# Kernel tuning notes

Measured on AMD Instinct MI355X. Metric: run time of the kernel, lower is better.

## Reference

```python
import jax, jax.numpy as jnp
import numpy as np

B, S, H = 8, 512, 768
NH, DH = 12, 64
I = 3072
E = 8
TOPK = 2
EPS = 1e-12


def _ln(x, g, b):
    m = jnp.mean(x, axis=-1, keepdims=True)
    v = jnp.mean(jnp.square(x - m), axis=-1, keepdims=True)
    return (x - m) * jax.lax.rsqrt(v + EPS) * g + b


def setup_inputs() -> dict:
    key = jax.random.key(0)
    ks = jax.random.split(key, 20)
    s_h = 1.0 / np.sqrt(H)
    s_i = 1.0 / np.sqrt(I)
    inp = {
        "hidden_states": jax.random.normal(ks[0], (B, S, H), jnp.float32),
        "Wq": jax.random.normal(ks[1], (H, H), jnp.float32) * s_h,
        "bq": jnp.zeros((H,), jnp.float32),
        "Wk": jax.random.normal(ks[2], (H, H), jnp.float32) * s_h,
        "bk": jnp.zeros((H,), jnp.float32),
        "Wv": jax.random.normal(ks[3], (H, H), jnp.float32) * s_h,
        "bv": jnp.zeros((H,), jnp.float32),
        "Wo": jax.random.normal(ks[4], (H, H), jnp.float32) * s_h,
        "bo": jnp.zeros((H,), jnp.float32),
        "ln_attn_g": jnp.ones((H,), jnp.float32),
        "ln_attn_b": jnp.zeros((H,), jnp.float32),
        "ln_ffn_g": jnp.ones((H,), jnp.float32),
        "ln_ffn_b": jnp.zeros((H,), jnp.float32),
        "Wr": jax.random.normal(ks[5], (H, E), jnp.float32) * s_h,
        "br": jnp.zeros((E,), jnp.float32),
        "W_up": jax.random.normal(ks[6], (E, H, I), jnp.float32) * s_h,
        "b_up": jnp.zeros((E, I), jnp.float32),
        "W_new": jax.random.normal(ks[7], (E, H, I), jnp.float32) * s_h,
        "b_new": jnp.zeros((E, I), jnp.float32),
        "W_down": jax.random.normal(ks[8], (E, I, H), jnp.float32) * s_i,
        "b_down": jnp.zeros((E, H), jnp.float32),
    }
    return inp


def reference(hidden_states, Wq, bq, Wk, bk, Wv, bv, Wo, bo,
              ln_attn_g, ln_attn_b, ln_ffn_g, ln_ffn_b,
              Wr, br, W_up, b_up, W_new, b_new, W_down, b_down):
    x = hidden_states
    # --- BertSelfAttention ---
    q = (x @ Wq + bq).reshape(B, S, NH, DH).transpose(0, 2, 1, 3)
    k = (x @ Wk + bk).reshape(B, S, NH, DH).transpose(0, 2, 1, 3)
    v = (x @ Wv + bv).reshape(B, S, NH, DH).transpose(0, 2, 1, 3)
    scores = jnp.einsum("bhqd,bhkd->bhqk", q, k) / np.sqrt(DH)
    probs = jax.nn.softmax(scores, axis=-1)
    ctx = jnp.einsum("bhqk,bhkd->bhqd", probs, v)
    ctx = ctx.transpose(0, 2, 1, 3).reshape(B, S, H)
    # --- BertSelfOutput: dense + residual + LayerNorm ---
    attention_output = _ln(ctx @ Wo + bo + x, ln_attn_g, ln_attn_b)
    # --- feed_forward_chunk: LayerNorm then token top-k MoE ---
    xl = _ln(attention_output, ln_ffn_g, ln_ffn_b)
    router_logits = xl @ Wr + br                      # [B,S,E]
    router_probs = jax.nn.softmax(router_logits, axis=-1)
    topw, topi = jax.lax.top_k(router_probs, TOPK)    # [B,S,K]
    topw = topw / jnp.sum(topw, axis=-1, keepdims=True)
    gates = jnp.sum(jax.nn.one_hot(topi, E, dtype=xl.dtype) * topw[..., None], axis=-2)  # [B,S,E]
    # --- experts (BertExpert: gelu(up(x)) * new(x) -> down), dense over E ---
    up = jax.nn.gelu(jnp.einsum("bsh,ehi->ebsi", xl, W_up) + b_up[:, None, None, :], approximate=False)
    gate_h = jnp.einsum("bsh,ehi->ebsi", xl, W_new) + b_new[:, None, None, :]
    y = jnp.einsum("ebsi,eih->ebsh", up * gate_h, W_down) + b_down[:, None, None, :]
    moe_out = jnp.einsum("ebsh,bse->bsh", y, gates)
    layer_output = moe_out + attention_output
    return layer_output, router_logits
```

## Files before the change

### kernel.cpp

```cpp
#include <hip/hip_runtime.h>
#include <hip/hip_bf16.h>
#include <cmath>


constexpr int cB = 8, cS = 512, cH = 768, cNH = 12, cDH = 64, cI = 3072, cE = 8;
constexpr int cT = cB * cS;
constexpr size_t TH = (size_t)cT * cH;

typedef __hip_bfloat16 bf16;
typedef __attribute__((ext_vector_type(8))) short s8v;
typedef __attribute__((ext_vector_type(4))) float f4v;

constexpr size_t SZ_WEXP     = (size_t)cE * cI * cH / 2;
constexpr size_t OFF_WUP_T   = 0;
constexpr size_t OFF_WNEW_T  = OFF_WUP_T + SZ_WEXP;
constexpr size_t OFF_WDOWN_T = OFF_WNEW_T + SZ_WEXP;
constexpr size_t OFF_QKV     = OFF_WDOWN_T + SZ_WEXP;
constexpr size_t OFF_CTX     = OFF_QKV + 4 * TH;
constexpr size_t OFF_XLB     = OFF_CTX + TH;
constexpr size_t OFF_WGT     = OFF_XLB + TH / 2;
constexpr size_t OFF_COUNTS  = OFF_WGT + 2 * cT;
constexpr size_t OFF_LISTS   = OFF_COUNTS + 16;

__device__ __forceinline__ void glds16(const void* g, void* l) {
    __builtin_amdgcn_global_load_lds(
        (const __attribute__((address_space(1))) unsigned int*)g,
        (__attribute__((address_space(3))) unsigned int*)l, 16, 0, 0);
}

__global__ void init_counts_kernel(int* __restrict__ counts) {
    if (threadIdx.x < cE) counts[threadIdx.x] = 0;
}

__global__ __launch_bounds__(256) void transpose_bf16_kernel(
    const float* __restrict__ src, bf16* __restrict__ dst, int R, int C) {
    __shared__ float tile[64][65];
    const size_t zb = (size_t)blockIdx.z * R * C;
    const int r0 = blockIdx.y * 64, c0 = blockIdx.x * 64;
    const int t = threadIdx.x;
    const int lr = t >> 4, lc = (t & 15) * 4;
#pragma unroll
    for (int i = 0; i < 4; ++i) {
        float4 v = *(const float4*)(src + zb + (size_t)(r0 + lr + i * 16) * C + c0 + lc);
        tile[lr + i * 16][lc + 0] = v.x; tile[lr + i * 16][lc + 1] = v.y;
        tile[lr + i * 16][lc + 2] = v.z; tile[lr + i * 16][lc + 3] = v.w;
    }
    __syncthreads();
#pragma unroll
    for (int i = 0; i < 4; ++i) {
        int cr = lr + i * 16;
        bf16 o[4];
#pragma unroll
        for (int j = 0; j < 4; ++j) o[j] = (bf16)tile[lc + j][cr];
        *(uint2*)(dst + zb + (size_t)(c0 + cr) * R + r0 + lc) = *(uint2*)o;
    }
}

__device__ __forceinline__ void gemm_body(
    const float* __restrict__ A, const float* __restrict__ B,
    const float* __restrict__ bias, float* __restrict__ C,
    int N, int K, int m0, int n0) {
    __shared__ float As[16][65];
    __shared__ float Bs[16][64];
    const int tid = threadIdx.x;
    const int tx = tid & 15, ty = tid >> 4;
    const int ar = tid >> 2, ac = (tid & 3) * 4;
    const int br = tid >> 4, bc = (tid & 15) * 4;
    float acc[4][4] = {};
    for (int k0 = 0; k0 < K; k0 += 16) {
        float4 av = *(const float4*)(A + (size_t)(m0 + ar) * K + k0 + ac);
        As[ac + 0][ar] = av.x; As[ac + 1][ar] = av.y;
        As[ac + 2][ar] = av.z; As[ac + 3][ar] = av.w;
        *(float4*)&Bs[br][bc] = *(const float4*)(B + (size_t)(k0 + br) * N + n0 + bc);
        __syncthreads();
#pragma unroll
        for (int kk = 0; kk < 16; ++kk) {
            float a[4], bv[4];
#pragma unroll
            for (int i = 0; i < 4; ++i) a[i] = As[kk][ty * 4 + i];
            *(float4*)bv = *(const float4*)&Bs[kk][tx * 4];
#pragma unroll
            for (int i = 0; i < 4; ++i)
#pragma unroll
                for (int j = 0; j < 4; ++j) acc[i][j] += a[i] * bv[j];
        }
        __syncthreads();
    }
#pragma unroll
    for (int i = 0; i < 4; ++i) {
        float4 o;
        o.x = acc[i][0] + bias[n0 + tx * 4 + 0];
        o.y = acc[i][1] + bias[n0 + tx * 4 + 1];
        o.z = acc[i][2] + bias[n0 + tx * 4 + 2];
        o.w = acc[i][3] + bias[n0 + tx * 4 + 3];
        *(float4*)(C + (size_t)(m0 + ty * 4 + i) * N + n0 + tx * 4) = o;
    }
}

__global__ __launch_bounds__(256) void gemm_qkv_kernel(
    const float* __restrict__ A,
    const float* __restrict__ Wq, const float* __restrict__ Wk,
    const float* __restrict__ Wv,
    const float* __restrict__ bq, const float* __restrict__ bk,
    const float* __restrict__ bv,
    float* __restrict__ q, float* __restrict__ k, float* __restrict__ v) {
    const int z = blockIdx.z;
    const float* B = (z == 0) ? Wq : (z == 1) ? Wk : Wv;
    const float* bias = (z == 0) ? bq : (z == 1) ? bk : bv;
    float* C = (z == 0) ? q : (z == 1) ? k : v;
    gemm_body(A, B, bias, C, cH, cH, blockIdx.y * 64, blockIdx.x * 64);
}

__global__ __launch_bounds__(256) void gemm_bias_kernel(
    const float* __restrict__ A, const float* __restrict__ B,
    const float* __restrict__ bias, float* __restrict__ C,
    int M, int N, int K) {
    gemm_body(A, B, bias, C, N, K, blockIdx.y * 64, blockIdx.x * 64);
}

__global__ __launch_bounds__(256) void attn_kernel(
    const float* __restrict__ q, const float* __restrict__ k,
    const float* __restrict__ v, float* __restrict__ ctx) {
    __shared__ float sQ[64][68];
    __shared__ float sKV[64][68];
    __shared__ float sS[64][68];
    __shared__ float sM[64], sL[64], sAl[64];
    const int q0 = blockIdx.x * 64, h = blockIdx.y, b = blockIdx.z;
    const int t = threadIdx.x;
    const int lr = t >> 2, lq = (t & 3) * 16;
    {
        const float* gq = q + (size_t)(b * cS + q0 + lr) * cH + h * cDH + lq;
#pragma unroll
        for (int j = 0; j < 4; ++j) {
            float4 x = *(const float4*)(gq + j * 4);
            x.x *= 0.125f; x.y *= 0.125f; x.z *= 0.125f; x.w *= 0.125f;
            *(float4*)&sQ[lr][lq + j * 4] = x;
        }
    }
    if (t < 64) { sM[t] = -1e30f; sL[t] = 0.f; }

    const int c0 = t & 15, rr = (t >> 4) * 4;
    const int d4 = (t & 15) * 4, rp = (t >> 4) * 4;
    const int sr = t >> 2, sc = (t & 3) * 16;

    float4 o_acc[4];
#pragma unroll
    for (int i = 0; i < 4; ++i) o_acc[i] = make_float4(0.f, 0.f, 0.f, 0.f);

    for (int kt = 0; kt < 8; ++kt) {
        float4 kreg[4];
        {
            const float* gk = k + (size_t)(b * cS + kt * 64 + lr) * cH + h * cDH + lq;
#pragma unroll
            for (int j = 0; j < 4; ++j) kreg[j] = *(const float4*)(gk + j * 4);
        }
        __syncthreads();
#pragma unroll
        for (int j = 0; j < 4; ++j) *(float4*)&sKV[lr][lq + j * 4] = kreg[j];
        __syncthreads();
        float accS[4][4] = {};
#pragma unroll
        for (int d = 0; d < 64; d += 4) {
            float4 qv[4], kv[4];
#pragma unroll
            for (int i = 0; i < 4; ++i) qv[i] = *(const float4*)&sQ[rr + i][d];
#pragma unroll
            for (int j = 0; j < 4; ++j) kv[j] = *(const float4*)&sKV[c0 + 16 * j][d];
#pragma unroll
            for (int i = 0; i < 4; ++i)
#pragma unroll
                for (int j = 0; j < 4; ++j)
                    accS[i][j] += qv[i].x * kv[j].x + qv[i].y * kv[j].y +
                                  qv[i].z * kv[j].z + qv[i].w * kv[j].w;
        }
#pragma unroll
        for (int i = 0; i < 4; ++i)
#pragma unroll
            for (int j = 0; j < 4; ++j) sS[rr + i][c0 + 16 * j] = accS[i][j];
        float4 vreg[4];
        {
            const float* gv = v + (size_t)(b * cS + kt * 64 + lr) * cH + h * cDH + lq;
#pragma unroll
            for (int j = 0; j < 4; ++j) vreg[j] = *(const float4*)(gv + j * 4);
        }
        __syncthreads();
        {
            float4 s[4];
#pragma unroll
            for (int j = 0; j < 4; ++j) s[j] = *(const float4*)&sS[sr][sc + j * 4];
            float m = -1e30f;
#pragma unroll
            for (int j = 0; j < 4; ++j)
                m = fmaxf(m, fmaxf(fmaxf(s[j].x, s[j].y), fmaxf(s[j].z, s[j].w)));
            m = fmaxf(m, __shfl_xor(m, 1));
            m = fmaxf(m, __shfl_xor(m, 2));
            float m_old = sM[sr];
            float m_new = fmaxf(m_old, m);
            float sum = 0.f;
#pragma unroll
            for (int j = 0; j < 4; ++j) {
                s[j].x = __expf(s[j].x - m_new); s[j].y = __expf(s[j].y - m_new);
                s[j].z = __expf(s[j].z - m_new); s[j].w = __expf(s[j].w - m_new);
                sum += s[j].x + s[j].y + s[j].z + s[j].w;
                *(float4*)&sS[sr][sc + j * 4] = s[j];
            }
            sum += __shfl_xor(sum, 1);
            sum += __shfl_xor(sum, 2);
            if ((t & 3) == 0) {
                float alpha = __expf(m_old - m_new);
                sAl[sr] = alpha;
                sM[sr] = m_new;
                sL[sr] = sL[sr] * alpha + sum;
            }
        }
#pragma unroll
        for (int j = 0; j < 4; ++j) *(float4*)&sKV[lr][lq + j * 4] = vreg[j];
        __syncthreads();
#pragma unroll
        for (int i = 0; i < 4; ++i) {
            float al = sAl[rp + i];
            o_acc[i].x *= al; o_acc[i].y *= al; o_acc[i].z *= al; o_acc[i].w *= al;
        }
        for (int kk4 = 0; kk4 < 64; kk4 += 4) {
            float4 pv[4], vv[4];
#pragma unroll
            for (int i = 0; i < 4; ++i) pv[i] = *(const float4*)&sS[rp + i][kk4];
#pragma unroll
            for (int j = 0; j < 4; ++j) vv[j] = *(const float4*)&sKV[kk4 + j][d4];
#pragma unroll
            for (int i = 0; i < 4; ++i) {
                o_acc[i].x += pv[i].x * vv[0].x + pv[i].y * vv[1].x +
                              pv[i].z * vv[2].x + pv[i].w * vv[3].x;
                o_acc[i].y += pv[i].x * vv[0].y + pv[i].y * vv[1].y +
                              pv[i].z * vv[2].y + pv[i].w * vv[3].y;
                o_acc[i].z += pv[i].x * vv[0].z + pv[i].y * vv[1].z +
                              pv[i].z * vv[2].z + pv[i].w * vv[3].z;
                o_acc[i].w += pv[i].x * vv[0].w + pv[i].y * vv[1].w +
                              pv[i].z * vv[2].w + pv[i].w * vv[3].w;
            }
        }
    }
    __syncthreads();
#pragma unroll
    for (int i = 0; i < 4; ++i) {
        float inv = 1.0f / sL[rp + i];
        float4 o = o_acc[i];
        o.x *= inv; o.y *= inv; o.z *= inv; o.w *= inv;
        *(float4*)(ctx + (size_t)(b * cS + q0 + rp + i) * cH + h * cDH + d4) = o;
    }
}

__device__ __forceinline__ float block_reduce_sum(float v, float* red) {
#pragma unroll
    for (int o = 32; o; o >>= 1) v += __shfl_xor(v, o);
    __syncthreads();
    if ((threadIdx.x & 63) == 0) red[threadIdx.x >> 6] = v;
    __syncthreads();
    return red[0] + red[1] + red[2] + red[3];
}

__global__ __launch_bounds__(256) void ln_router_kernel(
    const float* __restrict__ dense, const float* __restrict__ resid,
    const float* __restrict__ g1, const float* __restrict__ b1,
    const float* __restrict__ g2, const float* __restrict__ b2,
    const float* __restrict__ Wr, const float* __restrict__ br,
    float* __restrict__ out, bf16* __restrict__ xlb,
    float* __restrict__ out_logits, float* __restrict__ wgt,
    int* __restrict__ counts, int* __restrict__ lists) {
    __shared__ float red[4];
    __shared__ float lred[4][8];
    const int t = blockIdx.x, tid = threadIdx.x;
    const size_t base = (size_t)t * cH;
    float v[3], s = 0.f;
#pragma unroll
    for (int i = 0; i < 3; ++i) {
        v[i] = dense[base + tid + 256 * i] + resid[base + tid + 256 * i];
        s += v[i];
    }
    const float mean = block_reduce_sum(s, red) * (1.0f / cH);
    float vs = 0.f;
#pragma unroll
    for (int i = 0; i < 3; ++i) { float d = v[i] - mean; vs += d * d; }
    const float rstd = rsqrtf(block_reduce_sum(vs, red) * (1.0f / cH) + 1e-12f);
    float a[3], s2 = 0.f;
#pragma unroll
    for (int i = 0; i < 3; ++i) {
        a[i] = (v[i] - mean) * rstd * g1[tid + 256 * i] + b1[tid + 256 * i];
        out[base + tid + 256 * i] = a[i];
        s2 += a[i];
    }
    const float mean2 = block_reduce_sum(s2, red) * (1.0f / cH);
    float vs2 = 0.f;
#pragma unroll
    for (int i = 0; i < 3; ++i) { float d = a[i] - mean2; vs2 += d * d; }
    const float rstd2 = rsqrtf(block_reduce_sum(vs2, red) * (1.0f / cH) + 1e-12f);
    float xl[3];
#pragma unroll
    for (int i = 0; i < 3; ++i) {
        xl[i] = (a[i] - mean2) * rstd2 * g2[tid + 256 * i] + b2[tid + 256 * i];
        xlb[base + tid + 256 * i] = (bf16)xl[i];
    }
    float lg[cE] = {};
#pragma unroll
    for (int i = 0; i < 3; ++i) {
        const float* wr = Wr + (size_t)(tid + 256 * i) * cE;
#pragma unroll
        for (int e = 0; e < cE; ++e) lg[e] += xl[i] * wr[e];
    }
#pragma unroll
    for (int e = 0; e < cE; ++e)
#pragma unroll
        for (int o = 32; o; o >>= 1) lg[e] += __shfl_xor(lg[e], o);
    if ((tid & 63) == 0)
#pragma unroll
        for (int e = 0; e < cE; ++e) lred[tid >> 6][e] = lg[e];
    __syncthreads();
    if (tid == 0) {
        float logits[cE];
#pragma unroll
        for (int e = 0; e < cE; ++e) {
            logits[e] = lred[0][e] + lred[1][e] + lred[2][e] + lred[3][e] + br[e];
            out_logits[(size_t)t * cE + e] = logits[e];
        }
        int i0 = 0;
        for (int e = 1; e < cE; ++e) if (logits[e] > logits[i0]) i0 = e;
        int i1 = (i0 == 0) ? 1 : 0;
        for (int e = 0; e < cE; ++e)
            if (e != i0 && logits[e] > logits[i1]) i1 = e;
        float e1 = __expf(logits[i1] - logits[i0]);
        float w0 = 1.0f / (1.0f + e1);
        float w1 = e1 * w0;
        wgt[t * 2 + 0] = w0;
        wgt[t * 2 + 1] = w1;
        int p0 = atomicAdd(&counts[i0], 1);
        lists[i0 * cT + p0] = t * 2 + 0;
        int p1 = atomicAdd(&counts[i1], 1);
        lists[i1 * cT + p1] = t * 2 + 1;
    }
}

__global__ __launch_bounds__(256) void expert_up_mfma_kernel(
    const bf16* __restrict__ xlb,
    const bf16* __restrict__ WupT, const bf16* __restrict__ WnewT,
    const float* __restrict__ b_up, const float* __restrict__ b_new,
    const int* __restrict__ counts, const int* __restrict__ lists,
    bf16* __restrict__ act) {
    const int e = blockIdx.z;
    const int cnt = counts[e];
    const int m0 = blockIdx.y * 128;
    if (m0 >= cnt) return;
    const int n0 = blockIdx.x * 128;
    __shared__ short sA[128 * 32], sB1[128 * 32], sB2[128 * 32];
    __shared__ int rowa[128];
    const int t = threadIdx.x;
    if (t < 128) {
        int idx = m0 + t;
        rowa[t] = (idx < cnt) ? lists[e * cT + idx] : -1;
    }
    __syncthreads();
    const int lane = t & 63, w = t >> 6;
    const int wm = (w >> 1) * 64, wn = (w & 1) * 64;
    const int rA0 = t >> 2, kc8 = (t & 3) * 8;
    int a0 = rowa[rA0], a1 = rowa[rA0 + 64];
    const bf16* gA0 = xlb + (size_t)(a0 < 0 ? 0 : (a0 >> 1)) * cH + kc8;
    const bf16* gA1 = xlb + (size_t)(a1 < 0 ? 0 : (a1 >> 1)) * cH + kc8;
    const bf16* B1 = WupT + (size_t)e * cI * cH;
    const bf16* B2 = WnewT + (size_t)e * cI * cH;
    const bf16* gB10 = B1 + (size_t)(n0 + rA0) * cH + kc8;
    const bf16* gB11 = B1 + (size_t)(n0 + rA0 + 64) * cH + kc8;
    const bf16* gB20 = B2 + (size_t)(n0 + rA0) * cH + kc8;
    const bf16* gB21 = B2 + (size_t)(n0 + rA0 + 64) * cH + kc8;
    short* dA0  = sA  + t * 8;      short* dA1  = sA  + (t + 256) * 8;
    short* dB10 = sB1 + t * 8;      short* dB11 = sB1 + (t + 256) * 8;
    short* dB20 = sB2 + t * 8;      short* dB21 = sB2 + (t + 256) * 8;
    f4v zero = {0.f, 0.f, 0.f, 0.f};
    f4v acc1[4][4], acc2[4][4];
#pragma unroll
    for (int i = 0; i < 4; ++i)
#pragma unroll
        for (int j = 0; j < 4; ++j) { acc1[i][j] = zero; acc2[i][j] = zero; }
    const int fr = lane & 15, kg = (lane >> 4) * 8;
    for (int kk = 0; kk < cH; kk += 32) {
        glds16(gA0, dA0);   glds16(gA1, dA1);
        glds16(gB10, dB10); glds16(gB11, dB11);
        glds16(gB20, dB20); glds16(gB21, dB21);
        __syncthreads();
        s8v af[4], bf1[4], bf2[4];
#pragma unroll
        for (int i = 0; i < 4; ++i) {
            af[i]  = *(const s8v*)(sA  + (wm + i * 16 + fr) * 32 + kg);
            bf1[i] = *(const s8v*)(sB1 + (wn + i * 16 + fr) * 32 + kg);
            bf2[i] = *(const s8v*)(sB2 + (wn + i * 16 + fr) * 32 + kg);
        }
#pragma unroll
        for (int mi = 0; mi < 4; ++mi)
#pragma unroll
            for (int ni = 0; ni < 4; ++ni) {
                acc1[mi][ni] = __builtin_amdgcn_mfma_f32_16x16x32_bf16(
                    af[mi], bf1[ni], acc1[mi][ni], 0, 0, 0);
                acc2[mi][ni] = __builtin_amdgcn_mfma_f32_16x16x32_bf16(
                    af[mi], bf2[ni], acc2[mi][ni], 0, 0, 0);
            }
        __syncthreads();
        gA0 += 32; gA1 += 32; gB10 += 32; gB11 += 32; gB20 += 32; gB21 += 32;
    }
    const int cn = lane & 15, rq = (lane >> 4) * 4;
#pragma unroll
    for (int mi = 0; mi < 4; ++mi)
#pragma unroll
        for (int r = 0; r < 4; ++r) {
            int ml = wm + mi * 16 + rq + r;
            int a = rowa[ml];
            if (a < 0) continue;
            bf16* orow = act + (size_t)a * cI + n0 + wn;
#pragma unroll
            for (int ni = 0; ni < 4; ++ni) {
                int nl = ni * 16 + cn;
                float up = acc1[mi][ni][r] + b_up[e * cI + n0 + wn + nl];
                float nw = acc2[mi][ni][r] + b_new[e * cI + n0 + wn + nl];
                float g = 0.5f * up * (1.0f + erff(up * 0.70710678118654752f));
                orow[nl] = (bf16)(g * nw);
            }
        }
}

__global__ __launch_bounds__(256) void expert_down_mfma_kernel(
    const bf16* __restrict__ act, const bf16* __restrict__ WdownT,
    const float* __restrict__ b_down,
    const int* __restrict__ counts, const int* __restrict__ lists,
    const float* __restrict__ wgt, float* __restrict__ out) {
    const int e = blockIdx.z;
    const int cnt = counts[e];
    const int m0 = blockIdx.y * 128;
    if (m0 >= cnt) return;
    const int n0 = blockIdx.x * 128;
    __shared__ short sA[128 * 32], sB[128 * 32];
    __shared__ int rowa[128];
    const int t = threadIdx.x;
    if (t < 128) {
        int idx = m0 + t;
        rowa[t] = (idx < cnt) ? lists[e * cT + idx] : -1;
    }
    __syncthreads();
    const int lane = t & 63, w = t >> 6;
    const int wm = (w >> 1) * 64, wn = (w & 1) * 64;
    const int rA0 = t >> 2, kc8 = (t & 3) * 8;
    int a0 = rowa[rA0], a1 = rowa[rA0 + 64];
    const bf16* gA0 = act + (size_t)(a0 < 0 ? 0 : a0) * cI + kc8;
    const bf16* gA1 = act + (size_t)(a1 < 0 ? 0 : a1) * cI + kc8;
    const bf16* BT = WdownT + (size_t)e * cH * cI;
    const bf16* gB0 = BT + (size_t)(n0 + rA0) * cI + kc8;
    const bf16* gB1 = BT + (size_t)(n0 + rA0 + 64) * cI + kc8;
    short* dA0 = sA + t * 8;       short* dA1 = sA + (t + 256) * 8;
    short* dB0 = sB + t * 8;       short* dB1 = sB + (t + 256) * 8;
    f4v zero = {0.f, 0.f, 0.f, 0.f};
    f4v acc[4][4];
#pragma unroll
    for (int i = 0; i < 4; ++i)
#pragma unroll
        for (int j = 0; j < 4; ++j) acc[i][j] = zero;
    const int fr = lane & 15, kg = (lane >> 4) * 8;
    for (int kk = 0; kk < cI; kk += 32) {
        glds16(gA0, dA0); glds16(gA1, dA1);
        glds16(gB0, dB0); glds16(gB1, dB1);
        __syncthreads();
        s8v af[4], bf[4];
#pragma unroll
        for (int i = 0; i < 4; ++i) af[i] = *(const s8v*)(sA + (wm + i * 16 + fr) * 32 + kg);
#pragma unroll
        for (int i = 0; i < 4; ++i) bf[i] = *(const s8v*)(sB + (wn + i * 16 + fr) * 32 + kg);
#pragma unroll
        for (int mi = 0; mi < 4; ++mi)
#pragma unroll
            for (int ni = 0; ni < 4; ++ni)
                acc[mi][ni] = __builtin_amdgcn_mfma_f32_16x16x32_bf16(
                    af[mi], bf[ni], acc[mi][ni], 0, 0, 0);
        __syncthreads();
        gA0 += 32; gA1 += 32; gB0 += 32; gB1 += 32;
    }
    const int cn = lane & 15, rq = (lane >> 4) * 4;
#pragma unroll
    for (int mi = 0; mi < 4; ++mi)
#pragma unroll
        for (int r = 0; r < 4; ++r) {
            int ml = wm + mi * 16 + rq + r;
            int a = rowa[ml];
            if (a < 0) continue;
            int token = a >> 1;
            float wv = wgt[a];
#pragma unroll
            for (int ni = 0; ni < 4; ++ni) {
                int n = n0 + wn + ni * 16 + cn;
                atomicAdd(&out[(size_t)token * cH + n],
                          wv * (acc[mi][ni][r] + b_down[e * cH + n]));
            }
        }
}

extern "C" void kernel_launch(void* const* d_in, const int* in_sizes, int n_in,
                              void* d_out, int out_size, void* d_ws, size_t ws_size,
                              hipStream_t stream) {
    const float* x      = (const float*)d_in[0];
    const float* Wq     = (const float*)d_in[1];
    const float* bq     = (const float*)d_in[2];
    const float* Wk     = (const float*)d_in[3];
    const float* bk     = (const float*)d_in[4];
    const float* Wv     = (const float*)d_in[5];
    const float* bv     = (const float*)d_in[6];
    const float* Wo     = (const float*)d_in[7];
    const float* bo     = (const float*)d_in[8];
    const float* ln1g   = (const float*)d_in[9];
    const float* ln1b   = (const float*)d_in[10];
    const float* ln2g   = (const float*)d_in[11];
    const float* ln2b   = (const float*)d_in[12];
    const float* Wr     = (const float*)d_in[13];
    const float* br     = (const float*)d_in[14];
    const float* W_up   = (const float*)d_in[15];
    const float* b_up   = (const float*)d_in[16];
    const float* W_new  = (const float*)d_in[17];
    const float* b_new  = (const float*)d_in[18];
    const float* W_down = (const float*)d_in[19];
    const float* b_down = (const float*)d_in[20];

    float* out = (float*)d_out;
    float* ws  = (float*)d_ws;

    bf16* WupT   = (bf16*)(ws + OFF_WUP_T);
    bf16* WnewT  = (bf16*)(ws + OFF_WNEW_T);
    bf16* WdownT = (bf16*)(ws + OFF_WDOWN_T);
    float* q     = ws + OFF_QKV;
    float* k     = ws + OFF_QKV + TH;
    float* v     = ws + OFF_QKV + 2 * TH;
    float* tmp   = ws + OFF_QKV + 3 * TH;
    bf16* act    = (bf16*)(ws + OFF_QKV);
    float* ctx   = ws + OFF_CTX;
    bf16* xlb    = (bf16*)(ws + OFF_XLB);
    float* wgt   = ws + OFF_WGT;
    int* counts  = (int*)(ws + OFF_COUNTS);
    int* lists   = (int*)(ws + OFF_LISTS);

    init_counts_kernel<<<1, 64, 0, stream>>>(counts);

    transpose_bf16_kernel<<<dim3(48, 12, cE), 256, 0, stream>>>(W_up, WupT, cH, cI);
    transpose_bf16_kernel<<<dim3(48, 12, cE), 256, 0, stream>>>(W_new, WnewT, cH, cI);
    transpose_bf16_kernel<<<dim3(12, 48, cE), 256, 0, stream>>>(W_down, WdownT, cI, cH);

    gemm_qkv_kernel<<<dim3(cH / 64, cT / 64, 3), 256, 0, stream>>>(
        x, Wq, Wk, Wv, bq, bk, bv, q, k, v);
    attn_kernel<<<dim3(cS / 64, cNH, cB), 256, 0, stream>>>(q, k, v, ctx);
    gemm_bias_kernel<<<dim3(cH / 64, cT / 64), 256, 0, stream>>>(ctx, Wo, bo, tmp, cT, cH, cH);
    ln_router_kernel<<<cT, 256, 0, stream>>>(
        tmp, x, ln1g, ln1b, ln2g, ln2b, Wr, br,
        out, xlb, out + TH, wgt, counts, lists);

    expert_up_mfma_kernel<<<dim3(cI / 128, cT / 128, cE), 256, 0, stream>>>(
        xlb, WupT, WnewT, b_up, b_new, counts, lists, act);
    expert_down_mfma_kernel<<<dim3(cH / 128, cT / 128, cE), 256, 0, stream>>>(
        act, WdownT, b_down, counts, lists, wgt, out);
}
```

Baseline: 1.205 ms.

## Enlarge FP32 GEMM tiles to 128x128 and narrow expert-up N tile

The FP32 SIMT GEMM used for the QKV and output projections moves from 64x64 tiles with 4x4 per-thread outputs to 128x128 tiles with 8x8 per-thread outputs. Its B tile is now loaded directly into shared memory with the async global-to-LDS copy. The larger tiles raise arithmetic intensity and cut shared-memory traffic per FLOP, at the cost of more registers and fewer blocks (e.g. 6x32x3 for QKV). Separately, the expert up/new MFMA kernel halves its N tile to 64 to launch more blocks and lower accumulator register pressure, which means each A tile is fetched more often.

```diff
diff --git a/kernel.cpp b/kernel.cpp
--- a/kernel.cpp
+++ b/kernel.cpp
@@ -56,44 +56,58 @@
     }
 }
 
-__device__ __forceinline__ void gemm_body(
+__device__ __forceinline__ void gemm_body128(
     const float* __restrict__ A, const float* __restrict__ B,
     const float* __restrict__ bias, float* __restrict__ C,
     int N, int K, int m0, int n0) {
-    __shared__ float As[16][65];
-    __shared__ float Bs[16][64];
-    const int tid = threadIdx.x;
-    const int tx = tid & 15, ty = tid >> 4;
-    const int ar = tid >> 2, ac = (tid & 3) * 4;
-    const int br = tid >> 4, bc = (tid & 15) * 4;
-    float acc[4][4] = {};
+    __shared__ float As[16 * 132];
+    __shared__ float Bs[16 * 128];
+    const int t = threadIdx.x;
+    const int tx = t & 15, ty = t >> 4;
+    const int ar = t >> 2, ac = (t & 3) * 4;
+    const int bc = (t & 31) * 4, br = t >> 5;
+    const float* gB0 = B + (size_t)br * N + n0 + bc;
+    float* dB0 = Bs + t * 4;
+    float acc[8][8] = {};
     for (int k0 = 0; k0 < K; k0 += 16) {
-        float4 av = *(const float4*)(A + (size_t)(m0 + ar) * K + k0 + ac);
-        As[ac + 0][ar] = av.x; As[ac + 1][ar] = av.y;
-        As[ac + 2][ar] = av.z; As[ac + 3][ar] = av.w;
-        *(float4*)&Bs[br][bc] = *(const float4*)(B + (size_t)(k0 + br) * N + n0 + bc);
+        float4 a0 = *(const float4*)(A + (size_t)(m0 + ar) * K + k0 + ac);
+        float4 a1 = *(const float4*)(A + (size_t)(m0 + ar + 64) * K + k0 + ac);
+        glds16(gB0, dB0);
+        glds16(gB0 + (size_t)8 * N, dB0 + 1024);
+        As[(ac + 0) * 132 + ar] = a0.x; As[(ac + 1) * 132 + ar] = a0.y;
+        As[(ac + 2) * 132 + ar] = a0.z; As[(ac + 3) * 132 + ar] = a0.w;
+        As[(ac + 0) * 132 + ar + 64] = a1.x; As[(ac + 1) * 132 + ar + 64] = a1.y;
+        As[(ac + 2) * 132 + ar + 64] = a1.z; As[(ac + 3) * 132 + ar + 64] = a1.w;
         __syncthreads();
 #pragma unroll
         for (int kk = 0; kk < 16; ++kk) {
-            float a[4], bv[4];
-#pragma unroll
-            for (int i = 0; i < 4; ++i) a[i] = As[kk][ty * 4 + i];
-            *(float4*)bv = *(const float4*)&Bs[kk][tx * 4];
-#pragma unroll
-            for (int i = 0; i < 4; ++i)
-#pragma unroll
-                for (int j = 0; j < 4; ++j) acc[i][j] += a[i] * bv[j];
-        }
-        __syncthreads();
-    }
-#pragma unroll
-    for (int i = 0; i < 4; ++i) {
-        float4 o;
-        o.x = acc[i][0] + bias[n0 + tx * 4 + 0];
-        o.y = acc[i][1] + bias[n0 + tx * 4 + 1];
-        o.z = acc[i][2] + bias[n0 + tx * 4 + 2];
-        o.w = acc[i][3] + bias[n0 + tx * 4 + 3];
-        *(float4*)(C + (size_t)(m0 + ty * 4 + i) * N + n0 + tx * 4) = o;
+            float a[8], b[8];
+            *(float4*)&a[0] = *(const float4*)&As[kk * 132 + ty * 8];
+            *(float4*)&a[4] = *(const float4*)&As[kk * 132 + ty * 8 + 4];
+            *(float4*)&b[0] = *(const float4*)&Bs[kk * 128 + tx * 4];
+            *(float4*)&b[4] = *(const float4*)&Bs[kk * 128 + tx * 4 + 64];
+#pragma unroll
+            for (int i = 0; i < 8; ++i)
+#pragma unroll
+                for (int j = 0; j < 8; ++j) acc[i][j] += a[i] * b[j];
+        }
+        __syncthreads();
+        gB0 += (size_t)16 * N;
+    }
+#pragma unroll
+    for (int i = 0; i < 8; ++i) {
+        int m = m0 + ty * 8 + i;
+        float4 o0, o1;
+        o0.x = acc[i][0] + bias[n0 + tx * 4 + 0];
+        o0.y = acc[i][1] + bias[n0 + tx * 4 + 1];
+        o0.z = acc[i][2] + bias[n0 + tx * 4 + 2];
+        o0.w = acc[i][3] + bias[n0 + tx * 4 + 3];
+        o1.x = acc[i][4] + bias[n0 + 64 + tx * 4 + 0];
+        o1.y = acc[i][5] + bias[n0 + 64 + tx * 4 + 1];
+        o1.z = acc[i][6] + bias[n0 + 64 + tx * 4 + 2];
+        o1.w = acc[i][7] + bias[n0 + 64 + tx * 4 + 3];
+        *(float4*)(C + (size_t)m * N + n0 + tx * 4) = o0;
+        *(float4*)(C + (size_t)m * N + n0 + 64 + tx * 4) = o1;
     }
 }
 
@@ -108,14 +122,14 @@
     const float* B = (z == 0) ? Wq : (z == 1) ? Wk : Wv;
     const float* bias = (z == 0) ? bq : (z == 1) ? bk : bv;
     float* C = (z == 0) ? q : (z == 1) ? k : v;
-    gemm_body(A, B, bias, C, cH, cH, blockIdx.y * 64, blockIdx.x * 64);
+    gemm_body128(A, B, bias, C, cH, cH, blockIdx.y * 128, blockIdx.x * 128);
 }
 
 __global__ __launch_bounds__(256) void gemm_bias_kernel(
     const float* __restrict__ A, const float* __restrict__ B,
     const float* __restrict__ bias, float* __restrict__ C,
     int M, int N, int K) {
-    gemm_body(A, B, bias, C, N, K, blockIdx.y * 64, blockIdx.x * 64);
+    gemm_body128(A, B, bias, C, N, K, blockIdx.y * 128, blockIdx.x * 128);
 }
 
 __global__ __launch_bounds__(256) void attn_kernel(
@@ -138,11 +152,9 @@
         }
     }
     if (t < 64) { sM[t] = -1e30f; sL[t] = 0.f; }
-
     const int c0 = t & 15, rr = (t >> 4) * 4;
     const int d4 = (t & 15) * 4, rp = (t >> 4) * 4;
     const int sr = t >> 2, sc = (t & 3) * 16;
-
     float4 o_acc[4];
 #pragma unroll
     for (int i = 0; i < 4; ++i) o_acc[i] = make_float4(0.f, 0.f, 0.f, 0.f);
@@ -349,8 +361,8 @@
     const int cnt = counts[e];
     const int m0 = blockIdx.y * 128;
     if (m0 >= cnt) return;
-    const int n0 = blockIdx.x * 128;
-    __shared__ short sA[128 * 32], sB1[128 * 32], sB2[128 * 32];
+    const int n0 = blockIdx.x * 64;
+    __shared__ short sA[128 * 32], sB1[64 * 32], sB2[64 * 32];
     __shared__ int rowa[128];
     const int t = threadIdx.x;
     if (t < 128) {
@@ -359,50 +371,48 @@
     }
     __syncthreads();
     const int lane = t & 63, w = t >> 6;
-    const int wm = (w >> 1) * 64, wn = (w & 1) * 64;
+    const int wm = (w >> 1) * 64, wn = (w & 1) * 32;
     const int rA0 = t >> 2, kc8 = (t & 3) * 8;
     int a0 = rowa[rA0], a1 = rowa[rA0 + 64];
     const bf16* gA0 = xlb + (size_t)(a0 < 0 ? 0 : (a0 >> 1)) * cH + kc8;
     const bf16* gA1 = xlb + (size_t)(a1 < 0 ? 0 : (a1 >> 1)) * cH + kc8;
     const bf16* B1 = WupT + (size_t)e * cI * cH;
     const bf16* B2 = WnewT + (size_t)e * cI * cH;
-    const bf16* gB10 = B1 + (size_t)(n0 + rA0) * cH + kc8;
-    const bf16* gB11 = B1 + (size_t)(n0 + rA0 + 64) * cH + kc8;
-    const bf16* gB20 = B2 + (size_t)(n0 + rA0) * cH + kc8;
-    const bf16* gB21 = B2 + (size_t)(n0 + rA0 + 64) * cH + kc8;
-    short* dA0  = sA  + t * 8;      short* dA1  = sA  + (t + 256) * 8;
-    short* dB10 = sB1 + t * 8;      short* dB11 = sB1 + (t + 256) * 8;
-    short* dB20 = sB2 + t * 8;      short* dB21 = sB2 + (t + 256) * 8;
+    const bf16* gB1 = B1 + (size_t)(n0 + rA0) * cH + kc8;
+    const bf16* gB2 = B2 + (size_t)(n0 + rA0) * cH + kc8;
+    short* dA0 = sA + t * 8;   short* dA1 = sA + (t + 256) * 8;
+    short* dB1 = sB1 + t * 8;  short* dB2 = sB2 + t * 8;
     f4v zero = {0.f, 0.f, 0.f, 0.f};
-    f4v acc1[4][4], acc2[4][4];
+    f4v acc1[4][2], acc2[4][2];
 #pragma unroll
     for (int i = 0; i < 4; ++i)
 #pragma unroll
-        for (int j = 0; j < 4; ++j) { acc1[i][j] = zero; acc2[i][j] = zero; }
+        for (int j = 0; j < 2; ++j) { acc1[i][j] = zero; acc2[i][j] = zero; }
     const int fr = lane & 15, kg = (lane >> 4) * 8;
     for (int kk = 0; kk < cH; kk += 32) {
-        glds16(gA0, dA0);   glds16(gA1, dA1);
-        glds16(gB10, dB10); glds16(gB11, dB11);
-        glds16(gB20, dB20); glds16(gB21, dB21);
-        __syncthreads();
-        s8v af[4], bf1[4], bf2[4];
-#pragma unroll
-        for (int i = 0; i < 4; ++i) {
-            af[i]  = *(const s8v*)(sA  + (wm + i * 16 + fr) * 32 + kg);
-            bf1[i] = *(const s8v*)(sB1 + (wn + i * 16 + fr) * 32 + kg);
-            bf2[i] = *(const s8v*)(sB2 + (wn + i * 16 + fr) * 32 + kg);
+        glds16(gA0, dA0); glds16(gA1, dA1);
+        glds16(gB1, dB1); glds16(gB2, dB2);
+        __syncthreads();
+        s8v af[4], bf1[2], bf2[2];
+#pragma unroll
+        for (int i = 0; i < 4; ++i)
+            af[i] = *(const s8v*)(sA + (wm + i * 16 + fr) * 32 + kg);
+#pragma unroll
+        for (int j = 0; j < 2; ++j) {
+            bf1[j] = *(const s8v*)(sB1 + (wn + j * 16 + fr) * 32 + kg);
+            bf2[j] = *(const s8v*)(sB2 + (wn + j * 16 + fr) * 32 + kg);
         }
 #pragma unroll
         for (int mi = 0; mi < 4; ++mi)
 #pragma unroll
-            for (int ni = 0; ni < 4; ++ni) {
+            for (int ni = 0; ni < 2; ++ni) {
                 acc1[mi][ni] = __builtin_amdgcn_mfma_f32_16x16x32_bf16(
                     af[mi], bf1[ni], acc1[mi][ni], 0, 0, 0);
                 acc2[mi][ni] = __builtin_amdgcn_mfma_f32_16x16x32_bf16(
                     af[mi], bf2[ni], acc2[mi][ni], 0, 0, 0);
             }
         __syncthreads();
-        gA0 += 32; gA1 += 32; gB10 += 32; gB11 += 32; gB20 += 32; gB21 += 32;
+        gA0 += 32; gA1 += 32; gB1 += 32; gB2 += 32;
     }
     const int cn = lane & 15, rq = (lane >> 4) * 4;
 #pragma unroll
@@ -414,7 +424,7 @@
             if (a < 0) continue;
             bf16* orow = act + (size_t)a * cI + n0 + wn;
 #pragma unroll
-            for (int ni = 0; ni < 4; ++ni) {
+            for (int ni = 0; ni < 2; ++ni) {
                 int nl = ni * 16 + cn;
                 float up = acc1[mi][ni][r] + b_up[e * cI + n0 + wn + nl];
                 float nw = acc2[mi][ni][r] + b_new[e * cI + n0 + wn + nl];
@@ -545,15 +555,15 @@
     transpose_bf16_kernel<<<dim3(48, 12, cE), 256, 0, stream>>>(W_new, WnewT, cH, cI);
     transpose_bf16_kernel<<<dim3(12, 48, cE), 256, 0, stream>>>(W_down, WdownT, cI, cH);
 
-    gemm_qkv_kernel<<<dim3(cH / 64, cT / 64, 3), 256, 0, stream>>>(
+    gemm_qkv_kernel<<<dim3(cH / 128, cT / 128, 3), 256, 0, stream>>>(
         x, Wq, Wk, Wv, bq, bk, bv, q, k, v);
     attn_kernel<<<dim3(cS / 64, cNH, cB), 256, 0, stream>>>(q, k, v, ctx);
-    gemm_bias_kernel<<<dim3(cH / 64, cT / 64), 256, 0, stream>>>(ctx, Wo, bo, tmp, cT, cH, cH);
+    gemm_bias_kernel<<<dim3(cH / 128, cT / 128), 256, 0, stream>>>(ctx, Wo, bo, tmp, cT, cH, cH);
     ln_router_kernel<<<cT, 256, 0, stream>>>(
         tmp, x, ln1g, ln1b, ln2g, ln2b, Wr, br,
         out, xlb, out + TH, wgt, counts, lists);
 
-    expert_up_mfma_kernel<<<dim3(cI / 128, cT / 128, cE), 256, 0, stream>>>(
+    expert_up_mfma_kernel<<<dim3(cI / 64, cT / 128, cE), 256, 0, stream>>>(
         xlb, WupT, WnewT, b_up, b_new, counts, lists, act);
     expert_down_mfma_kernel<<<dim3(cH / 128, cT / 128, cE), 256, 0, stream>>>(
         act, WdownT, b_down, counts, lists, wgt, out);
```

After: 1.093 ms. 1.1x faster.
